# Performance work log

Hardware: AMD Instinct MI355X
Metric: run time of the kernel (lower is better)

The kernel has to match this reference:

```python
import jax, jax.numpy as jnp
import numpy as np

N_NODES = 50000
N_EDGES = 800000
N_RELS = 65
D = 64
N_GRAPHS = 512


def setup_inputs() -> dict:
    key = jax.random.key(0)
    ks = jax.random.split(key, 20)
    inp = {
        "node_feats": jax.random.normal(ks[0], (N_NODES, D), dtype=jnp.float32),
        "etypes": jax.random.randint(ks[1], (N_EDGES,), 0, N_RELS),
        "src": jax.random.randint(ks[2], (N_EDGES,), 0, N_NODES),
        "dst": jax.random.randint(ks[3], (N_EDGES,), 0, N_NODES),
        "graph_ids": jnp.sort(jax.random.randint(ks[4], (N_NODES,), 0, N_GRAPHS)),
    }
    s = 1.0 / np.sqrt(D)
    # 3 RGCN layers: per-relation weights (basis with num_bases=num_rels == full) + bias
    for i, k in zip(range(1, 4), (ks[5], ks[6], ks[7])):
        inp[f"W_rel{i}"] = jax.random.normal(k, (N_RELS, D, D), dtype=jnp.float32) * s
        inp[f"b{i}"] = jnp.zeros((D,), dtype=jnp.float32)
    # 3 FC layers
    for i, k in zip(range(1, 4), (ks[8], ks[9], ks[10])):
        inp[f"fc_W{i}"] = jax.random.normal(k, (D, D), dtype=jnp.float32) * s
        inp[f"fc_b{i}"] = jnp.zeros((D,), dtype=jnp.float32)
    inp["pred_W"] = jax.random.normal(ks[11], (D, 2), dtype=jnp.float32) * s
    inp["pred_b"] = jnp.zeros((2,), dtype=jnp.float32)
    return inp


def _rgcn_layer(h, W, b, etypes, src, dst):
    # all-relation projection: [N, R, K]
    proj = jnp.einsum('nd,rdk->nrk', h, W)
    # per-edge gather of relation-specific message: [E, K]
    msg = proj[src, etypes]
    # scatter-sum into destination nodes
    agg = jax.ops.segment_sum(msg, dst, num_segments=h.shape[0])
    return jax.nn.relu(agg + b)


def reference(node_feats, etypes, src, dst, graph_ids,
              W_rel1, b1, W_rel2, b2, W_rel3, b3,
              fc_W1, fc_b1, fc_W2, fc_b2, fc_W3, fc_b3,
              pred_W, pred_b):
    h = node_feats
    h = _rgcn_layer(h, W_rel1, b1, etypes, src, dst)
    h = _rgcn_layer(h, W_rel2, b2, etypes, src, dst)
    h = _rgcn_layer(h, W_rel3, b3, etypes, src, dst)
    # sum-pool nodes per graph: [G, D]
    g = jax.ops.segment_sum(h, graph_ids, num_segments=N_GRAPHS)
    g = jax.nn.relu(g @ fc_W1 + fc_b1)
    g = jax.nn.relu(g @ fc_W2 + fc_b2)
    g = jax.nn.relu(g @ fc_W3 + fc_b3)
    return g @ pred_W + pred_b
```

## Files before the change

### kernel.cpp

```cpp
#include <hip/hip_runtime.h>
#include <hip/hip_bf16.h>

#define N_NODES 50000
#define N_EDGES 800000
#define N_RELS 65
#define DIM 64
#define N_GRAPHS 512

#define SORT_BLOCKS 2048
#define CHUNK ((N_EDGES + SORT_BLOCKS - 1) / SORT_BLOCKS)

#define SCAN_BLK 512
#define NSCAN_BLKS ((N_NODES + SCAN_BLK - 1) / SCAN_BLK)

#define MSG_BLOCKS 2048
#define NWAVES (MSG_BLOCKS * 4)

typedef __attribute__((ext_vector_type(8))) short short8;
typedef __attribute__((ext_vector_type(4))) float f32x4;


__global__ void conv_h_zero_kernel(const float* __restrict__ x, __hip_bfloat16* __restrict__ y,
                                   int* __restrict__ cnt_d, int* __restrict__ cnt_g) {
    int i = blockIdx.x * 256 + threadIdx.x;
    if (i < (N_NODES * DIM) / 4) {
        float4 v = *(const float4*)(x + (size_t)i * 4);
        unsigned short us[4];
        us[0] = __hip_bfloat16_raw(__float2bfloat16(v.x)).x;
        us[1] = __hip_bfloat16_raw(__float2bfloat16(v.y)).x;
        us[2] = __hip_bfloat16_raw(__float2bfloat16(v.z)).x;
        us[3] = __hip_bfloat16_raw(__float2bfloat16(v.w)).x;
        *(ushort4*)(y + (size_t)i * 4) = *(const ushort4*)us;
    }
    if (i < N_NODES) cnt_d[i] = 0;
    if (i < N_GRAPHS) cnt_g[i] = 0;
}


__global__ __launch_bounds__(256) void wconv_kernel(
    const float* __restrict__ W1, const float* __restrict__ W2,
    const float* __restrict__ W3,
    __hip_bfloat16* __restrict__ Wt1, __hip_bfloat16* __restrict__ Wt2,
    __hip_bfloat16* __restrict__ Wt3) {
    __shared__ float tile[64][65];
    int b = blockIdx.x;
    int which = b / N_RELS, r = b - which * N_RELS;
    const float* W = (which == 0) ? W1 : (which == 1) ? W2 : W3;
    __hip_bfloat16* Wt = (which == 0) ? Wt1 : (which == 1) ? Wt2 : Wt3;
    int t = threadIdx.x;
    for (int i = t; i < 4096; i += 256) {
        int row = i >> 6, col = i & 63;
        tile[row][col] = W[(size_t)r * 4096 + i];
    }
    __syncthreads();
    for (int i = t; i < 4096; i += 256) {
        int row = i >> 6, col = i & 63;
        Wt[(size_t)r * 4096 + i] = __float2bfloat16(tile[col][row]);
    }
}


__global__ __launch_bounds__(256) void hist_all_kernel(
    const int* __restrict__ et, const int* __restrict__ gid,
    int* __restrict__ blk_hist, int* __restrict__ cnt_g) {
    __shared__ int lh[N_RELS];
    int t = threadIdx.x, b = blockIdx.x;
    int gtid = b * 256 + t;
    if (t < N_RELS) lh[t] = 0;
    __syncthreads();
    int lo = b * CHUNK;
    int hi = lo + CHUNK; if (hi > N_EDGES) hi = N_EDGES;
    for (int i = lo + t; i < hi; i += 256)
        atomicAdd(&lh[et[i]], 1);
    for (int i = gtid; i < N_NODES; i += SORT_BLOCKS * 256)
        atomicAdd(&cnt_g[gid[i]], 1);
    __syncthreads();
    if (t < N_RELS) blk_hist[t * SORT_BLOCKS + b] = lh[t];
}


__global__ __launch_bounds__(256) void relscan_kernel(const int* __restrict__ blk_hist,
                                                      int* __restrict__ blk_off,
                                                      int* __restrict__ rel_tot) {
    __shared__ int wsum[4];
    int r = blockIdx.x;
    int t = threadIdx.x;
    int w = t >> 6, lane = t & 63;
    const int PER = SORT_BLOCKS / 256;
    int4 v0 = *(const int4*)(blk_hist + (size_t)r * SORT_BLOCKS + t * PER);
    int4 v1 = *(const int4*)(blk_hist + (size_t)r * SORT_BLOCKS + t * PER + 4);
    int vals[8] = {v0.x, v0.y, v0.z, v0.w, v1.x, v1.y, v1.z, v1.w};
    int s = 0;
    #pragma unroll
    for (int j = 0; j < 8; ++j) s += vals[j];
    int x = s;
    #pragma unroll
    for (int off = 1; off < 64; off <<= 1) {
        int y = __shfl_up(x, off);
        if (lane >= off) x += y;
    }
    if (lane == 63) wsum[w] = x;
    __syncthreads();
    int base = 0;
    for (int i = 0; i < w; ++i) base += wsum[i];
    int run = base + x - s;
    int out[8];
    #pragma unroll
    for (int j = 0; j < 8; ++j) { out[j] = run; run += vals[j]; }
    *(int4*)(blk_off + (size_t)r * SORT_BLOCKS + t * PER)     = *(const int4*)&out[0];
    *(int4*)(blk_off + (size_t)r * SORT_BLOCKS + t * PER + 4) = *(const int4*)&out[4];
    if (t == 255) rel_tot[r] = base + x;
}


__global__ __launch_bounds__(64) void reltop_kernel(const int* __restrict__ rel_tot,
                                                    int* __restrict__ rel_ptr,
                                                    int* __restrict__ tile_base) {
    if (threadIdx.x == 0) {
        int s = 0, tt = 0;
        for (int q = 0; q < N_RELS; ++q) {
            int v = rel_tot[q];
            rel_ptr[q] = s; s += v;
            tile_base[q] = tt; tt += (v + 15) >> 4;
        }
        rel_ptr[N_RELS] = N_EDGES;
        tile_base[N_RELS] = tt;
    }
}


__global__ __launch_bounds__(256) void scatter2_kernel(
    const int* __restrict__ et, const int* __restrict__ src,
    const int* __restrict__ dst, const int* __restrict__ blk_off,
    const int* __restrict__ rel_ptr,
    unsigned long long* __restrict__ epk, int* __restrict__ cnt_d) {
    __shared__ int cur[N_RELS];
    int t = threadIdx.x, b = blockIdx.x;
    if (t < N_RELS) cur[t] = blk_off[t * SORT_BLOCKS + b] + rel_ptr[t];
    __syncthreads();
    int lo = b * CHUNK;
    int hi = lo + CHUNK; if (hi > N_EDGES) hi = N_EDGES;

    bool val[4]; int rr[4], dd[4]; unsigned ss[4];
    #pragma unroll
    for (int k = 0; k < 4; ++k) {
        int i = lo + t + k * 256;
        val[k] = (i < hi);
        int ic = val[k] ? i : lo;
        rr[k] = et[ic]; dd[k] = dst[ic]; ss[k] = (unsigned)src[ic];
    }
    int p[4];
    #pragma unroll
    for (int k = 0; k < 4; ++k)
        if (val[k]) p[k] = atomicAdd(&cur[rr[k]], 1);
    int rk[4];
    #pragma unroll
    for (int k = 0; k < 4; ++k)
        if (val[k]) rk[k] = atomicAdd(&cnt_d[dd[k]], 1);
    #pragma unroll
    for (int k = 0; k < 4; ++k)
        if (val[k]) {
            unsigned lo32 = ss[k] | ((unsigned)dd[k] << 16);
            epk[p[k]] = (unsigned long long)lo32 |
                        ((unsigned long long)(unsigned)rk[k] << 32);
        }
}


__global__ __launch_bounds__(SCAN_BLK) void scanblk_kernel(const int* __restrict__ cnt,
                                                           int* __restrict__ outv,
                                                           int* __restrict__ blk_tot) {
    __shared__ int tmp[SCAN_BLK];
    int t = threadIdx.x;
    int i = blockIdx.x * SCAN_BLK + t;
    int v = (i < N_NODES) ? cnt[i] : 0;
    tmp[t] = v;
    __syncthreads();
    for (int off = 1; off < SCAN_BLK; off <<= 1) {
        int add = (t >= off) ? tmp[t - off] : 0;
        __syncthreads();
        tmp[t] += add;
        __syncthreads();
    }
    if (i < N_NODES) outv[i] = tmp[t] - v;
    if (t == SCAN_BLK - 1) blk_tot[blockIdx.x] = tmp[t];
}

__global__ __launch_bounds__(64) void scantop_gid_kernel(
    const int* __restrict__ blk_tot, int* __restrict__ blk_base,
    const int* __restrict__ cnt_g, int* __restrict__ g_ptr) {
    int lane = threadIdx.x;
    if (blockIdx.x == 0) {
        if (lane == 0) {
            int run = 0;
            for (int b = 0; b < NSCAN_BLKS; ++b) { blk_base[b] = run; run += blk_tot[b]; }
        }
    } else {
        int run = 0;
        for (int c = 0; c < N_GRAPHS; c += 64) {
            int v = cnt_g[c + lane];
            int x = v;
            #pragma unroll
            for (int off = 1; off < 64; off <<= 1) {
                int y = __shfl_up(x, off);
                if (lane >= off) x += y;
            }
            g_ptr[c + lane] = run + x - v;
            run += __shfl(x, 63);
        }
    }
}

__global__ __launch_bounds__(SCAN_BLK) void scanadd_kernel(int* __restrict__ outv,
                                                           const int* __restrict__ blk_base) {
    int i = blockIdx.x * SCAN_BLK + threadIdx.x;
    if (i < N_NODES) outv[i] += blk_base[blockIdx.x];
}

__global__ void unpack_kernel(const unsigned long long* __restrict__ epk,
                              const int* __restrict__ row_ptr,
                              int* __restrict__ src_s, int* __restrict__ dpos) {
    int i = blockIdx.x * 256 + threadIdx.x;
    if (i < N_EDGES) {
        unsigned long long e = epk[i];
        int s = (int)(e & 0xFFFFu);
        int d = (int)((e >> 16) & 0xFFFFu);
        int rank = (int)(e >> 32);
        src_s[i] = s;
        dpos[i] = rank + row_ptr[d];
    }
}


__device__ inline unsigned pack2bf(float x, float y) {
    unsigned short ux = __hip_bfloat16_raw(__float2bfloat16(x)).x;
    unsigned short uy = __hip_bfloat16_raw(__float2bfloat16(y)).x;
    return (unsigned)ux | ((unsigned)uy << 16);
}

__global__ __launch_bounds__(256) void msg_mfma_kernel(
    const __hip_bfloat16* __restrict__ hb, const __hip_bfloat16* __restrict__ Wt,
    const int* __restrict__ rel_ptr, const int* __restrict__ tile_base,
    const int* __restrict__ src_s, const int* __restrict__ dpos,
    __hip_bfloat16* __restrict__ msg) {
    int t = threadIdx.x;
    int w = t >> 6, lane = t & 63;
    int quad = lane >> 4, m16 = lane & 15;
    int wave = blockIdx.x * 4 + w;

    int ntiles = tile_base[N_RELS];
    int tpw = (ntiles + NWAVES - 1) / NWAVES;
    int T = wave * tpw;
    int T1 = T + tpw; if (T1 > ntiles) T1 = ntiles;
    if (T >= T1) return;

    int r = 0;
    while (T >= tile_base[r + 1]) ++r;

    while (T < T1) {
        int chunk_end = tile_base[r + 1]; if (chunk_end > T1) chunk_end = T1;
        int e_base = rel_ptr[r], t_base = tile_base[r];
        int seg_end = rel_ptr[r + 1];

        const __hip_bfloat16* Wr = Wt + (size_t)r * (DIM * DIM);
        short8 bf00 = *(const short8*)(Wr + (4 * m16)     * DIM + quad * 8);
        short8 bf01 = *(const short8*)(Wr + (4 * m16 + 1) * DIM + quad * 8);
        short8 bf02 = *(const short8*)(Wr + (4 * m16 + 2) * DIM + quad * 8);
        short8 bf03 = *(const short8*)(Wr + (4 * m16 + 3) * DIM + quad * 8);
        short8 bf10 = *(const short8*)(Wr + (4 * m16)     * DIM + 32 + quad * 8);
        short8 bf11 = *(const short8*)(Wr + (4 * m16 + 1) * DIM + 32 + quad * 8);
        short8 bf12 = *(const short8*)(Wr + (4 * m16 + 2) * DIM + 32 + quad * 8);
        short8 bf13 = *(const short8*)(Wr + (4 * m16 + 3) * DIM + 32 + quad * 8);

        auto loadidx = [&](int TT, int& sv, int& dp) {
            int TC = TT < chunk_end ? TT : chunk_end - 1;
            int i = e_base + (TC - t_base) * 16 + lane;
            if (i >= N_EDGES) i = N_EDGES - 1;
            sv = src_s[i]; dp = dpos[i];
        };
        auto gatherA = [&](int sv, short8& x0, short8& x1) {
            int s = __shfl(sv, m16);
            const __hip_bfloat16* hp = hb + (size_t)s * DIM + quad * 8;
            x0 = *(const short8*)hp;
            x1 = *(const short8*)(hp + 32);
        };

        int sv0, dp0, sv1, dp1, sv2, dp2;
        short8 a0c, a1c, a0n, a1n;
        loadidx(T,     sv0, dp0);
        loadidx(T + 1, sv1, dp1);
        gatherA(sv0, a0c, a1c);

        for (; T < chunk_end; ++T) {
            loadidx(T + 2, sv2, dp2);
            gatherA(sv1, a0n, a1n);

            int e0 = e_base + (T - t_base) * 16;
            int rows = seg_end - e0; if (rows > 16) rows = 16;

            f32x4 c0 = {0.f, 0.f, 0.f, 0.f}, c1 = c0, c2 = c0, c3 = c0;
            c0 = __builtin_amdgcn_mfma_f32_16x16x32_bf16(a0c, bf00, c0, 0, 0, 0);
            c1 = __builtin_amdgcn_mfma_f32_16x16x32_bf16(a0c, bf01, c1, 0, 0, 0);
            c2 = __builtin_amdgcn_mfma_f32_16x16x32_bf16(a0c, bf02, c2, 0, 0, 0);
            c3 = __builtin_amdgcn_mfma_f32_16x16x32_bf16(a0c, bf03, c3, 0, 0, 0);
            c0 = __builtin_amdgcn_mfma_f32_16x16x32_bf16(a1c, bf10, c0, 0, 0, 0);
            c1 = __builtin_amdgcn_mfma_f32_16x16x32_bf16(a1c, bf11, c1, 0, 0, 0);
            c2 = __builtin_amdgcn_mfma_f32_16x16x32_bf16(a1c, bf12, c2, 0, 0, 0);
            c3 = __builtin_amdgcn_mfma_f32_16x16x32_bf16(a1c, bf13, c3, 0, 0, 0);

            int dpr[4];
            #pragma unroll
            for (int g = 0; g < 4; ++g) dpr[g] = __shfl(dp0, quad * 4 + g);

            #pragma unroll
            for (int g = 0; g < 4; ++g) {
                if (quad * 4 + g < rows) {
                    uint2 pk;
                    pk.x = pack2bf(c0[g], c1[g]);
                    pk.y = pack2bf(c2[g], c3[g]);
                    *(uint2*)(msg + (size_t)dpr[g] * DIM + 4 * m16) = pk;
                }
            }

            sv0 = sv1; dp0 = dp1; sv1 = sv2; dp1 = dp2;
            a0c = a0n; a1c = a1n;
        }
        ++r;
        while (T < T1 && T >= tile_base[r + 1]) ++r;
    }
}


__global__ __launch_bounds__(256) void agg_kernel(
    const __hip_bfloat16* __restrict__ msg, const int* __restrict__ row_ptr,
    const int* __restrict__ cnt_d, const float* __restrict__ b,
    __hip_bfloat16* __restrict__ hout) {
    int wave = blockIdx.x * 4 + (threadIdx.x >> 6);
    int lane = threadIdx.x & 63;
    if (wave >= N_NODES) return;
    int j0 = row_ptr[wave];
    int n  = cnt_d[wave];
    int rgrp = lane >> 3, dgrp = lane & 7;

    float a[8] = {0.f, 0.f, 0.f, 0.f, 0.f, 0.f, 0.f, 0.f};
    for (int jj = 0; jj < n; jj += 8) {
        int row = jj + rgrp;
        if (row < n) {
            uint4 d = *(const uint4*)(msg + (size_t)(j0 + row) * DIM + dgrp * 8);
            a[0] += __uint_as_float(d.x << 16);
            a[1] += __uint_as_float(d.x & 0xffff0000u);
            a[2] += __uint_as_float(d.y << 16);
            a[3] += __uint_as_float(d.y & 0xffff0000u);
            a[4] += __uint_as_float(d.z << 16);
            a[5] += __uint_as_float(d.z & 0xffff0000u);
            a[6] += __uint_as_float(d.w << 16);
            a[7] += __uint_as_float(d.w & 0xffff0000u);
        }
    }
    #pragma unroll
    for (int i = 0; i < 8; ++i) {
        a[i] += __shfl_xor(a[i], 8);
        a[i] += __shfl_xor(a[i], 16);
        a[i] += __shfl_xor(a[i], 32);
    }
    if (rgrp == 0) {
        unsigned short us[8];
        #pragma unroll
        for (int i = 0; i < 8; ++i) {
            float v = a[i] + b[dgrp * 8 + i];
            us[i] = __hip_bfloat16_raw(__float2bfloat16(v > 0.f ? v : 0.f)).x;
        }
        *(uint4*)(hout + (size_t)wave * DIM + dgrp * 8) = *(const uint4*)us;
    }
}


__global__ __launch_bounds__(256) void poolfc_kernel(
    const __hip_bfloat16* __restrict__ h, const int* __restrict__ g_ptr,
    const int* __restrict__ cnt_g,
    const float* __restrict__ W1, const float* __restrict__ b1,
    const float* __restrict__ W2, const float* __restrict__ b2,
    const float* __restrict__ W3, const float* __restrict__ b3,
    const float* __restrict__ pW, const float* __restrict__ pb,
    float* __restrict__ out) {
    int wave = blockIdx.x * 4 + (threadIdx.x >> 6);
    int lane = threadIdx.x & 63;
    if (wave >= N_GRAPHS) return;
    int j0 = g_ptr[wave];
    int n  = cnt_g[wave];
    int rgrp = lane >> 3, dgrp = lane & 7;

    float a[8] = {0.f, 0.f, 0.f, 0.f, 0.f, 0.f, 0.f, 0.f};
    for (int jj = 0; jj < n; jj += 8) {
        int row = jj + rgrp;
        if (row < n) {
            uint4 d = *(const uint4*)(h + (size_t)(j0 + row) * DIM + dgrp * 8);
            a[0] += __uint_as_float(d.x << 16);
            a[1] += __uint_as_float(d.x & 0xffff0000u);
            a[2] += __uint_as_float(d.y << 16);
            a[3] += __uint_as_float(d.y & 0xffff0000u);
            a[4] += __uint_as_float(d.z << 16);
            a[5] += __uint_as_float(d.z & 0xffff0000u);
            a[6] += __uint_as_float(d.w << 16);
            a[7] += __uint_as_float(d.w & 0xffff0000u);
        }
    }
    #pragma unroll
    for (int i = 0; i < 8; ++i) {
        a[i] += __shfl_xor(a[i], 8);
        a[i] += __shfl_xor(a[i], 16);
        a[i] += __shfl_xor(a[i], 32);
    }
    float v;
    {
        float acc = b1[lane];
        #pragma unroll
        for (int o = 0; o < 8; ++o)
            #pragma unroll
            for (int q = 0; q < 8; ++q)
                acc += __shfl(a[o], q) * W1[(q * 8 + o) * DIM + lane];
        v = acc > 0.f ? acc : 0.f;
    }
    {
        float acc = b2[lane];
        #pragma unroll
        for (int d = 0; d < DIM; ++d)
            acc += __shfl(v, d) * W2[d * DIM + lane];
        v = acc > 0.f ? acc : 0.f;
    }
    {
        float acc = b3[lane];
        #pragma unroll
        for (int d = 0; d < DIM; ++d)
            acc += __shfl(v, d) * W3[d * DIM + lane];
        v = acc > 0.f ? acc : 0.f;
    }
    float p0 = v * pW[lane * 2 + 0];
    float p1 = v * pW[lane * 2 + 1];
    #pragma unroll
    for (int off = 32; off > 0; off >>= 1) {
        p0 += __shfl_down(p0, off);
        p1 += __shfl_down(p1, off);
    }
    if (lane == 0) {
        out[wave * 2 + 0] = p0 + pb[0];
        out[wave * 2 + 1] = p1 + pb[1];
    }
}


extern "C" void kernel_launch(void* const* d_in, const int* in_sizes, int n_in,
                              void* d_out, int out_size, void* d_ws, size_t ws_size,
                              hipStream_t stream) {
    const float* node_feats = (const float*)d_in[0];
    const int*   etypes     = (const int*)d_in[1];
    const int*   src        = (const int*)d_in[2];
    const int*   dst        = (const int*)d_in[3];
    const int*   graph_ids  = (const int*)d_in[4];
    const float* W1 = (const float*)d_in[5];
    const float* b1 = (const float*)d_in[6];
    const float* W2 = (const float*)d_in[7];
    const float* b2 = (const float*)d_in[8];
    const float* W3 = (const float*)d_in[9];
    const float* b3 = (const float*)d_in[10];
    const float* fcW1 = (const float*)d_in[11];
    const float* fcb1 = (const float*)d_in[12];
    const float* fcW2 = (const float*)d_in[13];
    const float* fcb2 = (const float*)d_in[14];
    const float* fcW3 = (const float*)d_in[15];
    const float* fcb3 = (const float*)d_in[16];
    const float* pW = (const float*)d_in[17];
    const float* pb = (const float*)d_in[18];
    float* out = (float*)d_out;

    char* p = (char*)d_ws;
    auto alloc = [&](size_t bytes) -> void* {
        void* r = (void*)p;
        p += (bytes + 255) & ~(size_t)255;
        return r;
    };
    int* blk_hist  = (int*)alloc((size_t)SORT_BLOCKS * N_RELS * sizeof(int));
    int* blk_off   = (int*)alloc((size_t)SORT_BLOCKS * N_RELS * sizeof(int));
    int* rel_ptr   = (int*)alloc((N_RELS + 1) * sizeof(int));
    int* rel_tot   = (int*)alloc(N_RELS * sizeof(int));
    int* tile_base = (int*)alloc((N_RELS + 1) * sizeof(int));
    unsigned long long* epk = (unsigned long long*)alloc((size_t)N_EDGES * sizeof(unsigned long long));
    int* src_s     = (int*)alloc((size_t)N_EDGES * sizeof(int));
    int* dpos      = (int*)alloc((size_t)N_EDGES * sizeof(int));
    int* cnt_d     = (int*)alloc((size_t)N_NODES * sizeof(int));
    int* row_ptr   = (int*)alloc((size_t)N_NODES * sizeof(int));
    int* blk_tot   = (int*)alloc(NSCAN_BLKS * sizeof(int));
    int* blk_base  = (int*)alloc(NSCAN_BLKS * sizeof(int));
    int* cnt_g     = (int*)alloc(N_GRAPHS * sizeof(int));
    int* g_ptr     = (int*)alloc(N_GRAPHS * sizeof(int));
    __hip_bfloat16* hb0 = (__hip_bfloat16*)alloc((size_t)N_NODES * DIM * sizeof(__hip_bfloat16));
    __hip_bfloat16* hb1 = (__hip_bfloat16*)alloc((size_t)N_NODES * DIM * sizeof(__hip_bfloat16));
    __hip_bfloat16* Wt1 = (__hip_bfloat16*)alloc((size_t)N_RELS * DIM * DIM * sizeof(__hip_bfloat16));
    __hip_bfloat16* Wt2 = (__hip_bfloat16*)alloc((size_t)N_RELS * DIM * DIM * sizeof(__hip_bfloat16));
    __hip_bfloat16* Wt3 = (__hip_bfloat16*)alloc((size_t)N_RELS * DIM * DIM * sizeof(__hip_bfloat16));
    __hip_bfloat16* msg = (__hip_bfloat16*)alloc((size_t)N_EDGES * DIM * sizeof(__hip_bfloat16));

    const int EBLK = (N_EDGES + 255) / 256;
    const int CBLK = (N_NODES * DIM / 4 + 255) / 256;
    const int AGG_BLOCKS = (N_NODES + 3) / 4;

    conv_h_zero_kernel<<<CBLK, 256, 0, stream>>>(node_feats, hb0, cnt_d, cnt_g);
    wconv_kernel<<<3 * N_RELS, 256, 0, stream>>>(W1, W2, W3, Wt1, Wt2, Wt3);
    hist_all_kernel<<<SORT_BLOCKS, 256, 0, stream>>>(etypes, graph_ids, blk_hist, cnt_g);
    relscan_kernel<<<N_RELS, 256, 0, stream>>>(blk_hist, blk_off, rel_tot);
    reltop_kernel<<<1, 64, 0, stream>>>(rel_tot, rel_ptr, tile_base);
    scatter2_kernel<<<SORT_BLOCKS, 256, 0, stream>>>(etypes, src, dst, blk_off, rel_ptr,
                                                     epk, cnt_d);
    scanblk_kernel<<<NSCAN_BLKS, SCAN_BLK, 0, stream>>>(cnt_d, row_ptr, blk_tot);
    scantop_gid_kernel<<<2, 64, 0, stream>>>(blk_tot, blk_base, cnt_g, g_ptr);
    scanadd_kernel<<<NSCAN_BLKS, SCAN_BLK, 0, stream>>>(row_ptr, blk_base);
    unpack_kernel<<<EBLK, 256, 0, stream>>>(epk, row_ptr, src_s, dpos);

    msg_mfma_kernel<<<MSG_BLOCKS, 256, 0, stream>>>(hb0, Wt1, rel_ptr, tile_base,
                                                    src_s, dpos, msg);
    agg_kernel<<<AGG_BLOCKS, 256, 0, stream>>>(msg, row_ptr, cnt_d, b1, hb1);

    msg_mfma_kernel<<<MSG_BLOCKS, 256, 0, stream>>>(hb1, Wt2, rel_ptr, tile_base,
                                                    src_s, dpos, msg);
    agg_kernel<<<AGG_BLOCKS, 256, 0, stream>>>(msg, row_ptr, cnt_d, b2, hb0);

    msg_mfma_kernel<<<MSG_BLOCKS, 256, 0, stream>>>(hb0, Wt3, rel_ptr, tile_base,
                                                    src_s, dpos, msg);
    agg_kernel<<<AGG_BLOCKS, 256, 0, stream>>>(msg, row_ptr, cnt_d, b3, hb1);

    poolfc_kernel<<<(N_GRAPHS + 3) / 4, 256, 0, stream>>>(hb1, g_ptr, cnt_g,
                                                          fcW1, fcb1, fcW2, fcb2,
                                                          fcW3, fcb3, pW, pb, out);
}
```

Measured before the change: 385.5 us.

## Move destination-rank atomics to unpack and halve sort block count

The scatter kernel no longer returns a per-edge rank from its cnt_d atomics. It only increments the counts and writes a 32-bit packed (src,dst) word instead of a 64-bit one. The rank is now taken in the unpack kernel through atomics on a second counter array, cnt_d2, which is zeroed alongside cnt_d. SORT_BLOCKS also drops from 2048 to 1024, and relscan now handles 4 entries per thread. The aim is less packed-edge traffic and more independent atomics in scatter, at the cost of a second atomic pass over 800K edges. In-segment order changes nondeterministically, which can alter the float summation order.

After: 411.6 us. 6.8% more time.

```diff
diff --git a/kernel.cpp b/kernel.cpp
--- a/kernel.cpp
+++ b/kernel.cpp
@@ -7,7 +7,7 @@
 #define DIM 64
 #define N_GRAPHS 512
 
-#define SORT_BLOCKS 2048
+#define SORT_BLOCKS 1024
 #define CHUNK ((N_EDGES + SORT_BLOCKS - 1) / SORT_BLOCKS)
 
 #define SCAN_BLK 512
@@ -21,7 +21,8 @@
 
 
 __global__ void conv_h_zero_kernel(const float* __restrict__ x, __hip_bfloat16* __restrict__ y,
-                                   int* __restrict__ cnt_d, int* __restrict__ cnt_g) {
+                                   int* __restrict__ cnt_d, int* __restrict__ cnt_d2,
+                                   int* __restrict__ cnt_g) {
     int i = blockIdx.x * 256 + threadIdx.x;
     if (i < (N_NODES * DIM) / 4) {
         float4 v = *(const float4*)(x + (size_t)i * 4);
@@ -32,7 +33,7 @@
         us[3] = __hip_bfloat16_raw(__float2bfloat16(v.w)).x;
         *(ushort4*)(y + (size_t)i * 4) = *(const ushort4*)us;
     }
-    if (i < N_NODES) cnt_d[i] = 0;
+    if (i < N_NODES) { cnt_d[i] = 0; cnt_d2[i] = 0; }
     if (i < N_GRAPHS) cnt_g[i] = 0;
 }
 
@@ -88,11 +89,10 @@
     int w = t >> 6, lane = t & 63;
     const int PER = SORT_BLOCKS / 256;
     int4 v0 = *(const int4*)(blk_hist + (size_t)r * SORT_BLOCKS + t * PER);
-    int4 v1 = *(const int4*)(blk_hist + (size_t)r * SORT_BLOCKS + t * PER + 4);
-    int vals[8] = {v0.x, v0.y, v0.z, v0.w, v1.x, v1.y, v1.z, v1.w};
+    int vals[4] = {v0.x, v0.y, v0.z, v0.w};
     int s = 0;
     #pragma unroll
-    for (int j = 0; j < 8; ++j) s += vals[j];
+    for (int j = 0; j < PER; ++j) s += vals[j];
     int x = s;
     #pragma unroll
     for (int off = 1; off < 64; off <<= 1) {
@@ -104,11 +104,10 @@
     int base = 0;
     for (int i = 0; i < w; ++i) base += wsum[i];
     int run = base + x - s;
-    int out[8];
-    #pragma unroll
-    for (int j = 0; j < 8; ++j) { out[j] = run; run += vals[j]; }
-    *(int4*)(blk_off + (size_t)r * SORT_BLOCKS + t * PER)     = *(const int4*)&out[0];
-    *(int4*)(blk_off + (size_t)r * SORT_BLOCKS + t * PER + 4) = *(const int4*)&out[4];
+    int out[4];
+    #pragma unroll
+    for (int j = 0; j < PER; ++j) { out[j] = run; run += vals[j]; }
+    *(int4*)(blk_off + (size_t)r * SORT_BLOCKS + t * PER) = *(const int4*)&out[0];
     if (t == 255) rel_tot[r] = base + x;
 }
 
@@ -133,7 +132,7 @@
     const int* __restrict__ et, const int* __restrict__ src,
     const int* __restrict__ dst, const int* __restrict__ blk_off,
     const int* __restrict__ rel_ptr,
-    unsigned long long* __restrict__ epk, int* __restrict__ cnt_d) {
+    unsigned* __restrict__ epk, int* __restrict__ cnt_d) {
     __shared__ int cur[N_RELS];
     int t = threadIdx.x, b = blockIdx.x;
     if (t < N_RELS) cur[t] = blk_off[t * SORT_BLOCKS + b] + rel_ptr[t];
@@ -149,21 +148,17 @@
         int ic = val[k] ? i : lo;
         rr[k] = et[ic]; dd[k] = dst[ic]; ss[k] = (unsigned)src[ic];
     }
+    #pragma unroll
+    for (int k = 0; k < 4; ++k)
+        if (val[k]) atomicAdd(&cnt_d[dd[k]], 1);
     int p[4];
     #pragma unroll
     for (int k = 0; k < 4; ++k)
         if (val[k]) p[k] = atomicAdd(&cur[rr[k]], 1);
-    int rk[4];
     #pragma unroll
     for (int k = 0; k < 4; ++k)
-        if (val[k]) rk[k] = atomicAdd(&cnt_d[dd[k]], 1);
-    #pragma unroll
-    for (int k = 0; k < 4; ++k)
-        if (val[k]) {
-            unsigned lo32 = ss[k] | ((unsigned)dd[k] << 16);
-            epk[p[k]] = (unsigned long long)lo32 |
-                        ((unsigned long long)(unsigned)rk[k] << 32);
-        }
+        if (val[k])
+            epk[p[k]] = ss[k] | ((unsigned)dd[k] << 16);
 }
 
 
@@ -217,15 +212,16 @@
     if (i < N_NODES) outv[i] += blk_base[blockIdx.x];
 }
 
-__global__ void unpack_kernel(const unsigned long long* __restrict__ epk,
+__global__ void unpack_kernel(const unsigned* __restrict__ epk,
                               const int* __restrict__ row_ptr,
+                              int* __restrict__ cnt_d2,
                               int* __restrict__ src_s, int* __restrict__ dpos) {
     int i = blockIdx.x * 256 + threadIdx.x;
     if (i < N_EDGES) {
-        unsigned long long e = epk[i];
+        unsigned e = epk[i];
         int s = (int)(e & 0xFFFFu);
-        int d = (int)((e >> 16) & 0xFFFFu);
-        int rank = (int)(e >> 32);
+        int d = (int)(e >> 16);
+        int rank = atomicAdd(&cnt_d2[d], 1);
         src_s[i] = s;
         dpos[i] = rank + row_ptr[d];
     }
@@ -484,10 +480,11 @@
     int* rel_ptr   = (int*)alloc((N_RELS + 1) * sizeof(int));
     int* rel_tot   = (int*)alloc(N_RELS * sizeof(int));
     int* tile_base = (int*)alloc((N_RELS + 1) * sizeof(int));
-    unsigned long long* epk = (unsigned long long*)alloc((size_t)N_EDGES * sizeof(unsigned long long));
+    unsigned* epk  = (unsigned*)alloc((size_t)N_EDGES * sizeof(unsigned));
     int* src_s     = (int*)alloc((size_t)N_EDGES * sizeof(int));
     int* dpos      = (int*)alloc((size_t)N_EDGES * sizeof(int));
     int* cnt_d     = (int*)alloc((size_t)N_NODES * sizeof(int));
+    int* cnt_d2    = (int*)alloc((size_t)N_NODES * sizeof(int));
     int* row_ptr   = (int*)alloc((size_t)N_NODES * sizeof(int));
     int* blk_tot   = (int*)alloc(NSCAN_BLKS * sizeof(int));
     int* blk_base  = (int*)alloc(NSCAN_BLKS * sizeof(int));
@@ -504,7 +501,7 @@
     const int CBLK = (N_NODES * DIM / 4 + 255) / 256;
     const int AGG_BLOCKS = (N_NODES + 3) / 4;
 
-    conv_h_zero_kernel<<<CBLK, 256, 0, stream>>>(node_feats, hb0, cnt_d, cnt_g);
+    conv_h_zero_kernel<<<CBLK, 256, 0, stream>>>(node_feats, hb0, cnt_d, cnt_d2, cnt_g);
     wconv_kernel<<<3 * N_RELS, 256, 0, stream>>>(W1, W2, W3, Wt1, Wt2, Wt3);
     hist_all_kernel<<<SORT_BLOCKS, 256, 0, stream>>>(etypes, graph_ids, blk_hist, cnt_g);
     relscan_kernel<<<N_RELS, 256, 0, stream>>>(blk_hist, blk_off, rel_tot);
@@ -514,7 +511,7 @@
     scanblk_kernel<<<NSCAN_BLKS, SCAN_BLK, 0, stream>>>(cnt_d, row_ptr, blk_tot);
     scantop_gid_kernel<<<2, 64, 0, stream>>>(blk_tot, blk_base, cnt_g, g_ptr);
     scanadd_kernel<<<NSCAN_BLKS, SCAN_BLK, 0, stream>>>(row_ptr, blk_base);
-    unpack_kernel<<<EBLK, 256, 0, stream>>>(epk, row_ptr, src_s, dpos);
+    unpack_kernel<<<EBLK, 256, 0, stream>>>(epk, row_ptr, cnt_d2, src_s, dpos);
 
     msg_mfma_kernel<<<MSG_BLOCKS, 256, 0, stream>>>(hb0, Wt1, rel_ptr, tile_base,
                                                     src_s, dpos, msg);
```

## Bin edges by relation in shared memory before scattering to global

Applied to the files above, without the earlier changes.

The relation-sort scatter kernel now does a local counting sort of each block's edges in shared memory. It uses a wave-level prefix scan of the per-block histogram, then writes each relation's run to global memory as a contiguous segment instead of one random 8-byte store per edge. The number of sort blocks is halved so each block handles about twice as many edges, which makes each per-relation run longer. The relation scan is adjusted to match. In exchange the kernel uses more shared memory and one extra barrier per block, and there are fewer blocks to spread the work.

Result: no change. 383.4 us (-0.5%).

```diff
diff --git a/kernel.cpp b/kernel.cpp
--- a/kernel.cpp
+++ b/kernel.cpp
@@ -7,7 +7,7 @@
 #define DIM 64
 #define N_GRAPHS 512
 
-#define SORT_BLOCKS 2048
+#define SORT_BLOCKS 1024
 #define CHUNK ((N_EDGES + SORT_BLOCKS - 1) / SORT_BLOCKS)
 
 #define SCAN_BLK 512
@@ -88,11 +88,10 @@
     int w = t >> 6, lane = t & 63;
     const int PER = SORT_BLOCKS / 256;
     int4 v0 = *(const int4*)(blk_hist + (size_t)r * SORT_BLOCKS + t * PER);
-    int4 v1 = *(const int4*)(blk_hist + (size_t)r * SORT_BLOCKS + t * PER + 4);
-    int vals[8] = {v0.x, v0.y, v0.z, v0.w, v1.x, v1.y, v1.z, v1.w};
+    int vals[4] = {v0.x, v0.y, v0.z, v0.w};
     int s = 0;
     #pragma unroll
-    for (int j = 0; j < 8; ++j) s += vals[j];
+    for (int j = 0; j < PER; ++j) s += vals[j];
     int x = s;
     #pragma unroll
     for (int off = 1; off < 64; off <<= 1) {
@@ -104,11 +103,10 @@
     int base = 0;
     for (int i = 0; i < w; ++i) base += wsum[i];
     int run = base + x - s;
-    int out[8];
-    #pragma unroll
-    for (int j = 0; j < 8; ++j) { out[j] = run; run += vals[j]; }
-    *(int4*)(blk_off + (size_t)r * SORT_BLOCKS + t * PER)     = *(const int4*)&out[0];
-    *(int4*)(blk_off + (size_t)r * SORT_BLOCKS + t * PER + 4) = *(const int4*)&out[4];
+    int out[4];
+    #pragma unroll
+    for (int j = 0; j < PER; ++j) { out[j] = run; run += vals[j]; }
+    *(int4*)(blk_off + (size_t)r * SORT_BLOCKS + t * PER) = *(const int4*)&out[0];
     if (t == 255) rel_tot[r] = base + x;
 }
 
@@ -131,39 +129,61 @@
 
 __global__ __launch_bounds__(256) void scatter2_kernel(
     const int* __restrict__ et, const int* __restrict__ src,
-    const int* __restrict__ dst, const int* __restrict__ blk_off,
-    const int* __restrict__ rel_ptr,
+    const int* __restrict__ dst, const int* __restrict__ blk_hist,
+    const int* __restrict__ blk_off, const int* __restrict__ rel_ptr,
     unsigned long long* __restrict__ epk, int* __restrict__ cnt_d) {
-    __shared__ int cur[N_RELS];
+    __shared__ unsigned long long buf[CHUNK];
+    __shared__ unsigned char relof[CHUNK];
+    __shared__ int loff[N_RELS + 1];
+    __shared__ int lcur[N_RELS];
+    __shared__ int gbase[N_RELS];
     int t = threadIdx.x, b = blockIdx.x;
-    if (t < N_RELS) cur[t] = blk_off[t * SORT_BLOCKS + b] + rel_ptr[t];
-    __syncthreads();
+
+    if (t < 64) {
+        int v = blk_hist[t * SORT_BLOCKS + b];
+        int x = v;
+        #pragma unroll
+        for (int off = 1; off < 64; off <<= 1) {
+            int y = __shfl_up(x, off);
+            if (t >= off) x += y;
+        }
+        loff[t] = x - v;
+        lcur[t] = x - v;
+        gbase[t] = rel_ptr[t] + blk_off[t * SORT_BLOCKS + b];
+        if (t == 63) { loff[64] = x; lcur[64] = x; }
+    } else if (t == 64) {
+        gbase[64] = rel_ptr[64] + blk_off[64 * SORT_BLOCKS + b];
+    }
+    __syncthreads();
+
     int lo = b * CHUNK;
     int hi = lo + CHUNK; if (hi > N_EDGES) hi = N_EDGES;
-
-    bool val[4]; int rr[4], dd[4]; unsigned ss[4];
+    int nloc = hi - lo;
+
     #pragma unroll
     for (int k = 0; k < 4; ++k) {
         int i = lo + t + k * 256;
-        val[k] = (i < hi);
-        int ic = val[k] ? i : lo;
-        rr[k] = et[ic]; dd[k] = dst[ic]; ss[k] = (unsigned)src[ic];
-    }
-    int p[4];
-    #pragma unroll
-    for (int k = 0; k < 4; ++k)
-        if (val[k]) p[k] = atomicAdd(&cur[rr[k]], 1);
-    int rk[4];
-    #pragma unroll
-    for (int k = 0; k < 4; ++k)
-        if (val[k]) rk[k] = atomicAdd(&cnt_d[dd[k]], 1);
-    #pragma unroll
-    for (int k = 0; k < 4; ++k)
-        if (val[k]) {
-            unsigned lo32 = ss[k] | ((unsigned)dd[k] << 16);
-            epk[p[k]] = (unsigned long long)lo32 |
-                        ((unsigned long long)(unsigned)rk[k] << 32);
-        }
+        if (i < hi) {
+            int r = et[i], d = dst[i];
+            unsigned s = (unsigned)src[i];
+            int rank = atomicAdd(&cnt_d[d], 1);
+            int pl = atomicAdd(&lcur[r], 1);
+            unsigned lo32 = s | ((unsigned)d << 16);
+            buf[pl] = (unsigned long long)lo32 |
+                      ((unsigned long long)(unsigned)rank << 32);
+            relof[pl] = (unsigned char)r;
+        }
+    }
+    __syncthreads();
+
+    #pragma unroll
+    for (int k = 0; k < 4; ++k) {
+        int i = t + k * 256;
+        if (i < nloc) {
+            int r = relof[i];
+            epk[gbase[r] + i - loff[r]] = buf[i];
+        }
+    }
 }
 
 
@@ -509,8 +529,8 @@
     hist_all_kernel<<<SORT_BLOCKS, 256, 0, stream>>>(etypes, graph_ids, blk_hist, cnt_g);
     relscan_kernel<<<N_RELS, 256, 0, stream>>>(blk_hist, blk_off, rel_tot);
     reltop_kernel<<<1, 64, 0, stream>>>(rel_tot, rel_ptr, tile_base);
-    scatter2_kernel<<<SORT_BLOCKS, 256, 0, stream>>>(etypes, src, dst, blk_off, rel_ptr,
-                                                     epk, cnt_d);
+    scatter2_kernel<<<SORT_BLOCKS, 256, 0, stream>>>(etypes, src, dst, blk_hist, blk_off,
+                                                     rel_ptr, epk, cnt_d);
     scanblk_kernel<<<NSCAN_BLKS, SCAN_BLK, 0, stream>>>(cnt_d, row_ptr, blk_tot);
     scantop_gid_kernel<<<2, 64, 0, stream>>>(blk_tot, blk_base, cnt_g, g_ptr);
     scanadd_kernel<<<NSCAN_BLKS, SCAN_BLK, 0, stream>>>(row_ptr, blk_base);
```
